# Kernel optimization log

Measured on AMD Instinct MI355X. Metric: run time of the kernel, lower is better.

Reference implementation:

```python
import jax, jax.numpy as jnp
import numpy as np

N_NODES = 50000
N_EDGES = 800000
IN_DIM = 100
HIDDEN = 16
N_CLASSES = 40


def setup_inputs() -> dict:
    key = jax.random.key(0)
    k1, k2, k3, k4, k5, k6 = jax.random.split(key, 6)
    features = jax.random.normal(k1, (N_NODES, IN_DIM), dtype=jnp.float32)
    edge_src = jax.random.randint(k2, (N_EDGES,), 0, N_NODES, dtype=jnp.int32)
    edge_dst = jax.random.randint(k3, (N_EDGES,), 0, N_NODES, dtype=jnp.int32)
    edge_vals = jax.random.uniform(k4, (N_EDGES,), dtype=jnp.float32)
    W1 = jax.random.uniform(k5, (IN_DIM, HIDDEN), dtype=jnp.float32)
    W2 = jax.random.uniform(k6, (HIDDEN, N_CLASSES), dtype=jnp.float32)
    return {"features": features, "edge_src": edge_src, "edge_dst": edge_dst,
            "edge_vals": edge_vals, "W1": W1, "W2": W2}


def _spmm(edge_src, edge_dst, edge_vals, x):
    # z = A @ x with A given as (dst, src, val) edge list; equivalent to the
    # partition-loop addmm accumulation in broadcast().
    msgs = edge_vals[:, None] * x[edge_src]            # [E, d]
    return jax.ops.segment_sum(msgs, edge_dst, num_segments=x.shape[0])


def reference(features, edge_src, edge_dst, edge_vals, W1, W2):
    h = jax.nn.relu(_spmm(edge_src, edge_dst, edge_vals, features) @ W1)  # [N, 16]
    out = _spmm(edge_src, edge_dst, edge_vals, h) @ W2                    # [N, C]
    return jax.nn.log_softmax(out, axis=1)
```

## Files before the change

kernel.cpp:

```cpp
#include <hip/hip_runtime.h>

#define N_NODES   50000
#define N_EDGES   800000
#define IN_DIM    100
#define HIDDEN    16
#define N_CLASSES 40

#define BSHIFT 6
#define NPB    64
#define NBKT   782
#define PB     256
#define EPB    3125
#define EPT    7
#define CAP    2048
#define GNODES 32
#define GEMMB  782

#define K1_LDS 33456

__global__ __launch_bounds__(512) void build_and_gemm(const int* __restrict__ src,
                                                      const int* __restrict__ dst,
                                                      const float* __restrict__ val,
                                                      const float* __restrict__ X,
                                                      const float* __restrict__ W,
                                                      int* __restrict__ BTt,
                                                      int2* __restrict__ binned,
                                                      float* __restrict__ Y) {
    __shared__ __align__(16) char smem[K1_LDS];
    const int tid = threadIdx.x;

    if (blockIdx.x < PB) {
        int*  cnt    = (int*)smem;
        int*  lcur   = (int*)(smem + 3200);
        int*  sd     = (int*)(smem + 6400);
        int2* staged = (int2*)(smem + 8448);
        const int b = blockIdx.x, e0 = b * EPB;

        for (int k = tid; k < NBKT; k += 512) cnt[k] = 0;
        __syncthreads();

        int pk[EPT], ps[EPT]; float pv[EPT];
#pragma unroll
        for (int q = 0; q < EPT; ++q) {
            const int i = tid + q * 512;
            if (i < EPB) {
                const int e = e0 + i;
                const int d = dst[e];
                pk[q] = d >> BSHIFT;
                ps[q] = src[e] | ((d & (NPB - 1)) << 16);
                pv[q] = val[e];
                atomicAdd(&cnt[pk[q]], 1);
            } else pk[q] = -1;
        }
        __syncthreads();

        const int k0 = 2 * tid, k1 = 2 * tid + 1;
        const int a  = (k0 < NBKT) ? cnt[k0] : 0;
        const int bb = (k1 < NBKT) ? cnt[k1] : 0;
        const int s  = a + bb;
        sd[tid] = s;
        __syncthreads();
        for (int off = 1; off < 512; off <<= 1) {
            const int u = (tid >= off) ? sd[tid - off] : 0;
            __syncthreads();
            sd[tid] += u;
            __syncthreads();
        }
        const int excl = sd[tid] - s;
        if (k0 < NBKT) { lcur[k0] = excl;     BTt[k0 * PB + b] = excl; }
        if (k1 < NBKT) { lcur[k1] = excl + a; BTt[k1 * PB + b] = excl + a; }
        if (tid == 0)  BTt[NBKT * PB + b] = EPB;
        __syncthreads();

#pragma unroll
        for (int q = 0; q < EPT; ++q) {
            if (pk[q] >= 0) {
                const int pos = atomicAdd(&lcur[pk[q]], 1);
                staged[pos] = make_int2(ps[q], __float_as_int(pv[q]));
            }
        }
        __syncthreads();

        for (int i = tid; i < EPB; i += 512)
            binned[e0 + i] = staged[i];
    } else {
        float* sX = (float*)smem;
        float* sW = (float*)(smem + 25600);
        const int b2   = blockIdx.x - PB;
        const int row0 = b2 * 64;
        const int nrows = min(64, N_NODES - row0);

        const float4* W4 = (const float4*)W;
        float4* sW4 = (float4*)sW;
        for (int i = tid; i < (IN_DIM * HIDDEN) / 4; i += 512) sW4[i] = W4[i];
        const float4* X4 = (const float4*)(X + (size_t)row0 * IN_DIM);
        float4* sX4 = (float4*)sX;
        const int nf4 = nrows * (IN_DIM / 4);
        for (int i = tid; i < nf4; i += 512) sX4[i] = X4[i];
        __syncthreads();

        const int r = tid >> 3, hh = tid & 7;
        if (r >= nrows) return;
        float2 acc = make_float2(0.f, 0.f);
        const float* xr = &sX[r * IN_DIM];
#pragma unroll
        for (int k = 0; k < IN_DIM; ++k) {
            const float xk = xr[k];
            const float2 w = *(const float2*)&sW[k * HIDDEN + hh * 2];
            acc.x = fmaf(xk, w.x, acc.x);
            acc.y = fmaf(xk, w.y, acc.y);
        }
        *(float2*)&Y[(size_t)(row0 + r) * HIDDEN + hh * 2] = acc;
    }
}

__global__ __launch_bounds__(256) void sort_gather(const int* __restrict__ BTt,
                                                   const int2* __restrict__ binned,
                                                   const float* __restrict__ Xin,
                                                   int2* __restrict__ sorted,
                                                   int2* __restrict__ meta,
                                                   float* __restrict__ Z) {
    __shared__ int2 raw[CAP];
    __shared__ int2 srt[CAP];
    __shared__ int  cnt[NPB];
    __shared__ int  cur[NPB];
    __shared__ int  wsum[4];
    const int tid = threadIdx.x, k = blockIdx.x;
    const int lane = tid & 63, w = tid >> 6;

    if (tid < NPB) cnt[tid] = 0;

    const int rs = BTt[k * PB + tid];
    const int re = BTt[(k + 1) * PB + tid];
    const int len = re - rs;
    int x = len;
#pragma unroll
    for (int d = 1; d < 64; d <<= 1) {
        const int y = __shfl_up(x, d, 64);
        if (lane >= d) x += y;
    }
    if (lane == 63) wsum[w] = x;
    __syncthreads();
    int add = 0;
    for (int i = 0; i < w; ++i) add += wsum[i];
    const int tot = wsum[0] + wsum[1] + wsum[2] + wsum[3];

    int o = add + x - len;
    const int2* rb = binned + (size_t)tid * EPB;
    for (int p = rs; p < re; ++p, ++o) raw[o] = rb[p];
    __syncthreads();

    for (int i = tid; i < tot; i += 256)
        atomicAdd(&cnt[(raw[i].x >> 16) & (NPB - 1)], 1);
    __syncthreads();

    if (tid < NPB) {
        const int v  = cnt[tid];
        const int vp = (v + 1) & ~1;
        int xx = vp;
#pragma unroll
        for (int d = 1; d < 64; d <<= 1) {
            const int y = __shfl_up(xx, d, 64);
            if (tid >= d) xx += y;
        }
        const int excl = xx - vp;
        cur[tid] = excl;
        const int node = k * NPB + tid;
        if (node < N_NODES) meta[node] = make_int2(k * CAP + excl, v);
        if (tid == NPB - 1) wsum[0] = xx;
    }
    __syncthreads();
    const int padTot = wsum[0];

    for (int i = tid; i < tot; i += 256) {
        const int2 e = raw[i];
        const int pos = atomicAdd(&cur[(e.x >> 16) & (NPB - 1)], 1);
        srt[pos] = make_int2(e.x & 0xFFFF, e.y);
    }
    __syncthreads();

    for (int i = tid; i < padTot; i += 256)
        sorted[(size_t)k * CAP + i] = srt[i];

    const int g = tid >> 2, q = tid & 3;
    const int node = k * NPB + g;
    if (node >= N_NODES) return;
    const int deg = cnt[g];
    const int beg = cur[g] - deg;
    const float4* X4 = (const float4*)Xin;
    float4 acc = make_float4(0.f, 0.f, 0.f, 0.f);
    for (int p = beg; p < beg + deg; ++p) {
        const int2 e = srt[p];
        const float v = __int_as_float(e.y);
        const float4 xv = X4[(size_t)e.x * 4 + q];
        acc.x = fmaf(v, xv.x, acc.x);
        acc.y = fmaf(v, xv.y, acc.y);
        acc.z = fmaf(v, xv.z, acc.z);
        acc.w = fmaf(v, xv.w, acc.w);
    }
    acc.x = fmaxf(acc.x, 0.f); acc.y = fmaxf(acc.y, 0.f);
    acc.z = fmaxf(acc.z, 0.f); acc.w = fmaxf(acc.w, 0.f);
    ((float4*)Z)[(size_t)node * 4 + q] = acc;
}

__global__ __launch_bounds__(256) void gather_out(const int2* __restrict__ meta,
                                                  const int2* __restrict__ sorted,
                                                  const float* __restrict__ X,
                                                  const float* __restrict__ W2,
                                                  float* __restrict__ out) {
    __shared__ float sW[HIDDEN * N_CLASSES];
    __shared__ float zt[GNODES * 17];
    const int tid = threadIdx.x;
    for (int i = tid; i < HIDDEN * N_CLASSES; i += 256) sW[i] = W2[i];

    const int g = tid >> 3, j = tid & 7;
    const int n = blockIdx.x * GNODES + g;

    float2 acc = make_float2(0.f, 0.f);
    if (n < N_NODES) {
        const int2 md = meta[n];
        const int beg = md.x, end = md.x + md.y;
        const float2* X2 = (const float2*)X;
        int p = beg;
        for (; p + 4 <= end; p += 4) {
            const int4 ea = *(const int4*)&sorted[p];
            const int4 eb = *(const int4*)&sorted[p + 2];
            const float2 x0 = X2[(size_t)ea.x * 8 + j];
            const float2 x1 = X2[(size_t)ea.z * 8 + j];
            const float2 x2 = X2[(size_t)eb.x * 8 + j];
            const float2 x3 = X2[(size_t)eb.z * 8 + j];
            const float v0 = __int_as_float(ea.y), v1 = __int_as_float(ea.w);
            const float v2 = __int_as_float(eb.y), v3 = __int_as_float(eb.w);
            acc.x = fmaf(v0, x0.x, acc.x); acc.y = fmaf(v0, x0.y, acc.y);
            acc.x = fmaf(v1, x1.x, acc.x); acc.y = fmaf(v1, x1.y, acc.y);
            acc.x = fmaf(v2, x2.x, acc.x); acc.y = fmaf(v2, x2.y, acc.y);
            acc.x = fmaf(v3, x3.x, acc.x); acc.y = fmaf(v3, x3.y, acc.y);
        }
        for (; p < end; ++p) {
            const int2 e = sorted[p];
            const float2 xv = X2[(size_t)e.x * 8 + j];
            const float v = __int_as_float(e.y);
            acc.x = fmaf(v, xv.x, acc.x); acc.y = fmaf(v, xv.y, acc.y);
        }
    }
    zt[g * 17 + j * 2]     = acc.x;
    zt[g * 17 + j * 2 + 1] = acc.y;
    __syncthreads();
    if (n >= N_NODES) return;

    float z[HIDDEN];
#pragma unroll
    for (int k = 0; k < HIDDEN; ++k) z[k] = zt[g * 17 + k];

    float o[5];
#pragma unroll
    for (int i = 0; i < 5; ++i) o[i] = 0.f;
#pragma unroll
    for (int k = 0; k < HIDDEN; ++k) {
        const float zk = z[k];
#pragma unroll
        for (int i = 0; i < 5; ++i)
            o[i] = fmaf(zk, sW[k * N_CLASSES + j * 5 + i], o[i]);
    }

    float m = o[0];
#pragma unroll
    for (int i = 1; i < 5; ++i) m = fmaxf(m, o[i]);
#pragma unroll
    for (int d = 1; d < 8; d <<= 1) m = fmaxf(m, __shfl_xor(m, d, 8));
    float se = 0.f;
#pragma unroll
    for (int i = 0; i < 5; ++i) se += __expf(o[i] - m);
#pragma unroll
    for (int d = 1; d < 8; d <<= 1) se += __shfl_xor(se, d, 8);
    const float lse = m + __logf(se);

    float* orow = out + (size_t)n * N_CLASSES + j * 5;
#pragma unroll
    for (int i = 0; i < 5; ++i) orow[i] = o[i] - lse;
}

extern "C" void kernel_launch(void* const* d_in, const int* in_sizes, int n_in,
                              void* d_out, int out_size, void* d_ws, size_t ws_size,
                              hipStream_t stream) {
    const float* features = (const float*)d_in[0];
    const int*   edge_src = (const int*)d_in[1];
    const int*   edge_dst = (const int*)d_in[2];
    const float* edge_val = (const float*)d_in[3];
    const float* W1       = (const float*)d_in[4];
    const float* W2       = (const float*)d_in[5];
    float*       out      = (float*)d_out;

    char* base = (char*)d_ws;
    const size_t HNB = (size_t)N_NODES * HIDDEN * sizeof(float);
    float* y1     = (float*)(base);
    float* z1     = (float*)(base + HNB);
    int2*  binned = (int2*) (base + 2 * HNB);
    int2*  sortd  = (int2*) (base + 2 * HNB + (size_t)N_EDGES * 8);
    char*  tail   = base + 2 * HNB + (size_t)N_EDGES * 8
                         + (size_t)NBKT * CAP * 8;
    int*   BTt    = (int*) (tail);
    int2*  meta   = (int2*)(tail + (((size_t)(NBKT + 1) * PB * 4 + 255) & ~255ULL));

    build_and_gemm<<<PB + GEMMB, 512, 0, stream>>>(edge_src, edge_dst, edge_val,
                                                   features, W1, BTt, binned, y1);
    sort_gather<<<NBKT, 256, 0, stream>>>(BTt, binned, y1, sortd, meta, z1);
    gather_out<<<(N_NODES + GNODES - 1) / GNODES, 256, 0, stream>>>(meta, sortd, z1, W2, out);
}
```

Baseline: 125.6 us.

## Replace per-bucket counting sort with LDS atomic accumulation for both SpMM layers

Drops the second-level counting sort and the sorted/meta arrays. Each bucket block now reads its raw edges, and 16 lanes per edge accumulate v*x into a shared-memory accumulator with float atomics. The output layer reuses the same bucketed edge stream instead of re-reading a globally stored sorted list. The block-level prefix scan in the build kernel is also replaced with a wavefront shuffle scan. This removes the sort passes and the global writes and reads of the sorted edges, at the cost of LDS atomic contention and non-deterministic summation order.

Result: slower. 283.4 us (+125.7%).

```diff
diff --git a/kernel.cpp b/kernel.cpp
--- a/kernel.cpp
+++ b/kernel.cpp
@@ -13,7 +13,6 @@
 #define EPB    3125
 #define EPT    7
 #define CAP    2048
-#define GNODES 32
 #define GEMMB  782
 
 #define K1_LDS 33456
@@ -32,9 +31,10 @@
     if (blockIdx.x < PB) {
         int*  cnt    = (int*)smem;
         int*  lcur   = (int*)(smem + 3200);
-        int*  sd     = (int*)(smem + 6400);
+        int*  wpre   = (int*)(smem + 6400);
         int2* staged = (int2*)(smem + 8448);
         const int b = blockIdx.x, e0 = b * EPB;
+        const int lane = tid & 63, w = tid >> 6;
 
         for (int k = tid; k < NBKT; k += 512) cnt[k] = 0;
         __syncthreads();
@@ -58,15 +58,17 @@
         const int a  = (k0 < NBKT) ? cnt[k0] : 0;
         const int bb = (k1 < NBKT) ? cnt[k1] : 0;
         const int s  = a + bb;
-        sd[tid] = s;
-        __syncthreads();
-        for (int off = 1; off < 512; off <<= 1) {
-            const int u = (tid >= off) ? sd[tid - off] : 0;
-            __syncthreads();
-            sd[tid] += u;
-            __syncthreads();
-        }
-        const int excl = sd[tid] - s;
+        int x = s;
+#pragma unroll
+        for (int d = 1; d < 64; d <<= 1) {
+            const int y = __shfl_up(x, d, 64);
+            if (lane >= d) x += y;
+        }
+        if (lane == 63) wpre[w] = x;
+        __syncthreads();
+        int add = 0;
+        for (int i = 0; i < w; ++i) add += wpre[i];
+        const int excl = add + x - s;
         if (k0 < NBKT) { lcur[k0] = excl;     BTt[k0 * PB + b] = excl; }
         if (k1 < NBKT) { lcur[k1] = excl + a; BTt[k1 * PB + b] = excl + a; }
         if (tid == 0)  BTt[NBKT * PB + b] = EPB;
@@ -106,29 +108,30 @@
 #pragma unroll
         for (int k = 0; k < IN_DIM; ++k) {
             const float xk = xr[k];
-            const float2 w = *(const float2*)&sW[k * HIDDEN + hh * 2];
-            acc.x = fmaf(xk, w.x, acc.x);
-            acc.y = fmaf(xk, w.y, acc.y);
+            const float2 wv = *(const float2*)&sW[k * HIDDEN + hh * 2];
+            acc.x = fmaf(xk, wv.x, acc.x);
+            acc.y = fmaf(xk, wv.y, acc.y);
         }
         *(float2*)&Y[(size_t)(row0 + r) * HIDDEN + hh * 2] = acc;
     }
 }
 
-__global__ __launch_bounds__(256) void sort_gather(const int* __restrict__ BTt,
-                                                   const int2* __restrict__ binned,
-                                                   const float* __restrict__ Xin,
-                                                   int2* __restrict__ sorted,
-                                                   int2* __restrict__ meta,
-                                                   float* __restrict__ Z) {
-    __shared__ int2 raw[CAP];
-    __shared__ int2 srt[CAP];
-    __shared__ int  cnt[NPB];
-    __shared__ int  cur[NPB];
-    __shared__ int  wsum[4];
+template <bool IS_OUT>
+__global__ __launch_bounds__(256) void spmm_bucket2(const int* __restrict__ BTt,
+                                                    const int2* __restrict__ binned,
+                                                    const float* __restrict__ X,
+                                                    const float* __restrict__ W2,
+                                                    float* __restrict__ outp) {
+    __shared__ int2  raw[CAP];
+    __shared__ float acc[NPB * HIDDEN];
+    __shared__ int   wpre[4];
+    __shared__ float sW[HIDDEN * N_CLASSES];
     const int tid = threadIdx.x, k = blockIdx.x;
     const int lane = tid & 63, w = tid >> 6;
 
-    if (tid < NPB) cnt[tid] = 0;
+    for (int i = tid; i < NPB * HIDDEN; i += 256) acc[i] = 0.f;
+    if (IS_OUT)
+        for (int i = tid; i < HIDDEN * N_CLASSES; i += 256) sW[i] = W2[i];
 
     const int rs = BTt[k * PB + tid];
     const int re = BTt[(k + 1) * PB + tid];
@@ -139,145 +142,66 @@
         const int y = __shfl_up(x, d, 64);
         if (lane >= d) x += y;
     }
-    if (lane == 63) wsum[w] = x;
+    if (lane == 63) wpre[w] = x;
     __syncthreads();
     int add = 0;
-    for (int i = 0; i < w; ++i) add += wsum[i];
-    const int tot = wsum[0] + wsum[1] + wsum[2] + wsum[3];
+    for (int i = 0; i < w; ++i) add += wpre[i];
+    const int tot = wpre[0] + wpre[1] + wpre[2] + wpre[3];
 
     int o = add + x - len;
     const int2* rb = binned + (size_t)tid * EPB;
     for (int p = rs; p < re; ++p, ++o) raw[o] = rb[p];
     __syncthreads();
 
-    for (int i = tid; i < tot; i += 256)
-        atomicAdd(&cnt[(raw[i].x >> 16) & (NPB - 1)], 1);
+    const int j = tid & 15;
+    for (int i = tid >> 4; i < tot; i += 16) {
+        const int2 e = raw[i];
+        const int  sn = e.x & 0xFFFF;
+        const int  n  = (e.x >> 16) & (NPB - 1);
+        const float v = __int_as_float(e.y);
+        const float xv = X[(size_t)sn * HIDDEN + j];
+        unsafeAtomicAdd(&acc[n * HIDDEN + j], v * xv);
+    }
     __syncthreads();
 
-    if (tid < NPB) {
-        const int v  = cnt[tid];
-        const int vp = (v + 1) & ~1;
-        int xx = vp;
-#pragma unroll
-        for (int d = 1; d < 64; d <<= 1) {
-            const int y = __shfl_up(xx, d, 64);
-            if (tid >= d) xx += y;
-        }
-        const int excl = xx - vp;
-        cur[tid] = excl;
-        const int node = k * NPB + tid;
-        if (node < N_NODES) meta[node] = make_int2(k * CAP + excl, v);
-        if (tid == NPB - 1) wsum[0] = xx;
-    }
-    __syncthreads();
-    const int padTot = wsum[0];
-
-    for (int i = tid; i < tot; i += 256) {
-        const int2 e = raw[i];
-        const int pos = atomicAdd(&cur[(e.x >> 16) & (NPB - 1)], 1);
-        srt[pos] = make_int2(e.x & 0xFFFF, e.y);
-    }
-    __syncthreads();
-
-    for (int i = tid; i < padTot; i += 256)
-        sorted[(size_t)k * CAP + i] = srt[i];
-
-    const int g = tid >> 2, q = tid & 3;
-    const int node = k * NPB + g;
-    if (node >= N_NODES) return;
-    const int deg = cnt[g];
-    const int beg = cur[g] - deg;
-    const float4* X4 = (const float4*)Xin;
-    float4 acc = make_float4(0.f, 0.f, 0.f, 0.f);
-    for (int p = beg; p < beg + deg; ++p) {
-        const int2 e = srt[p];
-        const float v = __int_as_float(e.y);
-        const float4 xv = X4[(size_t)e.x * 4 + q];
-        acc.x = fmaf(v, xv.x, acc.x);
-        acc.y = fmaf(v, xv.y, acc.y);
-        acc.z = fmaf(v, xv.z, acc.z);
-        acc.w = fmaf(v, xv.w, acc.w);
-    }
-    acc.x = fmaxf(acc.x, 0.f); acc.y = fmaxf(acc.y, 0.f);
-    acc.z = fmaxf(acc.z, 0.f); acc.w = fmaxf(acc.w, 0.f);
-    ((float4*)Z)[(size_t)node * 4 + q] = acc;
-}
-
-__global__ __launch_bounds__(256) void gather_out(const int2* __restrict__ meta,
-                                                  const int2* __restrict__ sorted,
-                                                  const float* __restrict__ X,
-                                                  const float* __restrict__ W2,
-                                                  float* __restrict__ out) {
-    __shared__ float sW[HIDDEN * N_CLASSES];
-    __shared__ float zt[GNODES * 17];
-    const int tid = threadIdx.x;
-    for (int i = tid; i < HIDDEN * N_CLASSES; i += 256) sW[i] = W2[i];
-
-    const int g = tid >> 3, j = tid & 7;
-    const int n = blockIdx.x * GNODES + g;
-
-    float2 acc = make_float2(0.f, 0.f);
-    if (n < N_NODES) {
-        const int2 md = meta[n];
-        const int beg = md.x, end = md.x + md.y;
-        const float2* X2 = (const float2*)X;
-        int p = beg;
-        for (; p + 4 <= end; p += 4) {
-            const int4 ea = *(const int4*)&sorted[p];
-            const int4 eb = *(const int4*)&sorted[p + 2];
-            const float2 x0 = X2[(size_t)ea.x * 8 + j];
-            const float2 x1 = X2[(size_t)ea.z * 8 + j];
-            const float2 x2 = X2[(size_t)eb.x * 8 + j];
-            const float2 x3 = X2[(size_t)eb.z * 8 + j];
-            const float v0 = __int_as_float(ea.y), v1 = __int_as_float(ea.w);
-            const float v2 = __int_as_float(eb.y), v3 = __int_as_float(eb.w);
-            acc.x = fmaf(v0, x0.x, acc.x); acc.y = fmaf(v0, x0.y, acc.y);
-            acc.x = fmaf(v1, x1.x, acc.x); acc.y = fmaf(v1, x1.y, acc.y);
-            acc.x = fmaf(v2, x2.x, acc.x); acc.y = fmaf(v2, x2.y, acc.y);
-            acc.x = fmaf(v3, x3.x, acc.x); acc.y = fmaf(v3, x3.y, acc.y);
-        }
-        for (; p < end; ++p) {
-            const int2 e = sorted[p];
-            const float2 xv = X2[(size_t)e.x * 8 + j];
-            const float v = __int_as_float(e.y);
-            acc.x = fmaf(v, xv.x, acc.x); acc.y = fmaf(v, xv.y, acc.y);
-        }
-    }
-    zt[g * 17 + j * 2]     = acc.x;
-    zt[g * 17 + j * 2 + 1] = acc.y;
-    __syncthreads();
-    if (n >= N_NODES) return;
-
-    float z[HIDDEN];
-#pragma unroll
-    for (int k = 0; k < HIDDEN; ++k) z[k] = zt[g * 17 + k];
-
-    float o[5];
-#pragma unroll
-    for (int i = 0; i < 5; ++i) o[i] = 0.f;
-#pragma unroll
-    for (int k = 0; k < HIDDEN; ++k) {
-        const float zk = z[k];
-#pragma unroll
-        for (int i = 0; i < 5; ++i)
-            o[i] = fmaf(zk, sW[k * N_CLASSES + j * 5 + i], o[i]);
-    }
-
-    float m = o[0];
-#pragma unroll
-    for (int i = 1; i < 5; ++i) m = fmaxf(m, o[i]);
-#pragma unroll
-    for (int d = 1; d < 8; d <<= 1) m = fmaxf(m, __shfl_xor(m, d, 8));
-    float se = 0.f;
-#pragma unroll
-    for (int i = 0; i < 5; ++i) se += __expf(o[i] - m);
-#pragma unroll
-    for (int d = 1; d < 8; d <<= 1) se += __shfl_xor(se, d, 8);
-    const float lse = m + __logf(se);
-
-    float* orow = out + (size_t)n * N_CLASSES + j * 5;
-#pragma unroll
-    for (int i = 0; i < 5; ++i) orow[i] = o[i] - lse;
+    if (!IS_OUT) {
+        const int node = k * NPB + (tid >> 2);
+        if (node >= N_NODES) return;
+        float4 o4 = *(const float4*)&acc[tid * 4];
+        o4.x = fmaxf(o4.x, 0.f); o4.y = fmaxf(o4.y, 0.f);
+        o4.z = fmaxf(o4.z, 0.f); o4.w = fmaxf(o4.w, 0.f);
+        ((float4*)outp)[(size_t)node * 4 + (tid & 3)] = o4;
+    } else {
+        const int g = tid >> 2, q = tid & 3;
+        const int n = k * NPB + g;
+        if (n >= N_NODES) return;
+        float oc[10];
+#pragma unroll
+        for (int c = 0; c < 10; ++c) oc[c] = 0.f;
+        const float* zr = &acc[g * HIDDEN];
+#pragma unroll
+        for (int kk = 0; kk < HIDDEN; ++kk) {
+            const float zk = zr[kk];
+            const float* wr = &sW[kk * N_CLASSES + q * 10];
+#pragma unroll
+            for (int c = 0; c < 10; ++c) oc[c] = fmaf(zk, wr[c], oc[c]);
+        }
+        float m = oc[0];
+#pragma unroll
+        for (int c = 1; c < 10; ++c) m = fmaxf(m, oc[c]);
+#pragma unroll
+        for (int d = 1; d < 4; d <<= 1) m = fmaxf(m, __shfl_xor(m, d, 4));
+        float se = 0.f;
+#pragma unroll
+        for (int c = 0; c < 10; ++c) se += __expf(oc[c] - m);
+#pragma unroll
+        for (int d = 1; d < 4; d <<= 1) se += __shfl_xor(se, d, 4);
+        const float lse = m + __logf(se);
+
+        float* orow = outp + (size_t)n * N_CLASSES + q * 10;
+#pragma unroll
+        for (int c = 0; c < 10; ++c) orow[c] = oc[c] - lse;
+    }
 }
 
 extern "C" void kernel_launch(void* const* d_in, const int* in_sizes, int n_in,
@@ -296,14 +220,10 @@
     float* y1     = (float*)(base);
     float* z1     = (float*)(base + HNB);
     int2*  binned = (int2*) (base + 2 * HNB);
-    int2*  sortd  = (int2*) (base + 2 * HNB + (size_t)N_EDGES * 8);
-    char*  tail   = base + 2 * HNB + (size_t)N_EDGES * 8
-                         + (size_t)NBKT * CAP * 8;
-    int*   BTt    = (int*) (tail);
-    int2*  meta   = (int2*)(tail + (((size_t)(NBKT + 1) * PB * 4 + 255) & ~255ULL));
+    int*   BTt    = (int*)  (base + 2 * HNB + (size_t)N_EDGES * 8);
 
     build_and_gemm<<<PB + GEMMB, 512, 0, stream>>>(edge_src, edge_dst, edge_val,
                                                    features, W1, BTt, binned, y1);
-    sort_gather<<<NBKT, 256, 0, stream>>>(BTt, binned, y1, sortd, meta, z1);
-    gather_out<<<(N_NODES + GNODES - 1) / GNODES, 256, 0, stream>>>(meta, sortd, z1, W2, out);
+    spmm_bucket2<false><<<NBKT, 256, 0, stream>>>(BTt, binned, y1, nullptr, z1);
+    spmm_bucket2<true><<<NBKT, 256, 0, stream>>>(BTt, binned, z1, W2, out);
 }
```

## Use smaller binning blocks, warp-shuffle scan, and read binned edges directly in sort

Applied to the files above, without the earlier changes.

The edge-binning phase now runs 500 blocks of 256 threads over 1600 edges each instead of 256 blocks of 512, and the GEMM part uses 32-row tiles. The per-block bucket prefix sum moves from a shared-memory Hillis-Steele scan with many barriers to a wave-shuffle scan. sort_gather no longer stages raw edges in LDS; each thread reads its partition slices from global memory twice, for counting and for scattering, and the gather loop is unrolled by two. The aim is better occupancy and fewer barriers, at the cost of re-reading binned data from global memory and more BTt entries per bucket.

Measured after the change: 129.7 us. 3.3% more time.

```diff
diff --git a/kernel.cpp b/kernel.cpp
--- a/kernel.cpp
+++ b/kernel.cpp
@@ -9,16 +9,17 @@
 #define BSHIFT 6
 #define NPB    64
 #define NBKT   782
-#define PB     256
-#define EPB    3125
+#define PB     500
+#define EPB    1600
 #define EPT    7
 #define CAP    2048
+#define GROWS  32
+#define GEMMB  1563
 #define GNODES 32
-#define GEMMB  782
-
-#define K1_LDS 33456
-
-__global__ __launch_bounds__(512) void build_and_gemm(const int* __restrict__ src,
+
+#define K1_LDS 19264
+
+__global__ __launch_bounds__(256) void build_and_gemm(const int* __restrict__ src,
                                                       const int* __restrict__ dst,
                                                       const float* __restrict__ val,
                                                       const float* __restrict__ X,
@@ -32,17 +33,18 @@
     if (blockIdx.x < PB) {
         int*  cnt    = (int*)smem;
         int*  lcur   = (int*)(smem + 3200);
-        int*  sd     = (int*)(smem + 6400);
-        int2* staged = (int2*)(smem + 8448);
+        int*  wpre   = (int*)(smem + 6400);
+        int2* staged = (int2*)(smem + 6464);
         const int b = blockIdx.x, e0 = b * EPB;
-
-        for (int k = tid; k < NBKT; k += 512) cnt[k] = 0;
+        const int lane = tid & 63, w = tid >> 6;
+
+        for (int k = tid; k < NBKT; k += 256) cnt[k] = 0;
         __syncthreads();
 
         int pk[EPT], ps[EPT]; float pv[EPT];
 #pragma unroll
         for (int q = 0; q < EPT; ++q) {
-            const int i = tid + q * 512;
+            const int i = tid + q * 256;
             if (i < EPB) {
                 const int e = e0 + i;
                 const int d = dst[e];
@@ -54,22 +56,34 @@
         }
         __syncthreads();
 
-        const int k0 = 2 * tid, k1 = 2 * tid + 1;
-        const int a  = (k0 < NBKT) ? cnt[k0] : 0;
-        const int bb = (k1 < NBKT) ? cnt[k1] : 0;
-        const int s  = a + bb;
-        sd[tid] = s;
-        __syncthreads();
-        for (int off = 1; off < 512; off <<= 1) {
-            const int u = (tid >= off) ? sd[tid - off] : 0;
-            __syncthreads();
-            sd[tid] += u;
-            __syncthreads();
-        }
-        const int excl = sd[tid] - s;
-        if (k0 < NBKT) { lcur[k0] = excl;     BTt[k0 * PB + b] = excl; }
-        if (k1 < NBKT) { lcur[k1] = excl + a; BTt[k1 * PB + b] = excl + a; }
-        if (tid == 0)  BTt[NBKT * PB + b] = EPB;
+        int c[4], s = 0;
+#pragma unroll
+        for (int u = 0; u < 4; ++u) {
+            const int kk = 4 * tid + u;
+            c[u] = (kk < NBKT) ? cnt[kk] : 0;
+            s += c[u];
+        }
+        int x = s;
+#pragma unroll
+        for (int d = 1; d < 64; d <<= 1) {
+            const int y = __shfl_up(x, d, 64);
+            if (lane >= d) x += y;
+        }
+        if (lane == 63) wpre[w] = x;
+        __syncthreads();
+        int add = 0;
+        for (int i = 0; i < w; ++i) add += wpre[i];
+        int run = add + x - s;
+#pragma unroll
+        for (int u = 0; u < 4; ++u) {
+            const int kk = 4 * tid + u;
+            if (kk < NBKT) {
+                lcur[kk] = run;
+                BTt[kk * PB + b] = run;
+                run += c[u];
+            }
+        }
+        if (tid == 0) BTt[NBKT * PB + b] = EPB;
         __syncthreads();
 
 #pragma unroll
@@ -81,22 +95,22 @@
         }
         __syncthreads();
 
-        for (int i = tid; i < EPB; i += 512)
+        for (int i = tid; i < EPB; i += 256)
             binned[e0 + i] = staged[i];
     } else {
         float* sX = (float*)smem;
-        float* sW = (float*)(smem + 25600);
+        float* sW = (float*)(smem + 12800);
         const int b2   = blockIdx.x - PB;
-        const int row0 = b2 * 64;
-        const int nrows = min(64, N_NODES - row0);
+        const int row0 = b2 * GROWS;
+        const int nrows = min(GROWS, N_NODES - row0);
 
         const float4* W4 = (const float4*)W;
         float4* sW4 = (float4*)sW;
-        for (int i = tid; i < (IN_DIM * HIDDEN) / 4; i += 512) sW4[i] = W4[i];
+        for (int i = tid; i < (IN_DIM * HIDDEN) / 4; i += 256) sW4[i] = W4[i];
         const float4* X4 = (const float4*)(X + (size_t)row0 * IN_DIM);
         float4* sX4 = (float4*)sX;
         const int nf4 = nrows * (IN_DIM / 4);
-        for (int i = tid; i < nf4; i += 512) sX4[i] = X4[i];
+        for (int i = tid; i < nf4; i += 256) sX4[i] = X4[i];
         __syncthreads();
 
         const int r = tid >> 3, hh = tid & 7;
@@ -104,11 +118,11 @@
         float2 acc = make_float2(0.f, 0.f);
         const float* xr = &sX[r * IN_DIM];
 #pragma unroll
-        for (int k = 0; k < IN_DIM; ++k) {
-            const float xk = xr[k];
-            const float2 w = *(const float2*)&sW[k * HIDDEN + hh * 2];
-            acc.x = fmaf(xk, w.x, acc.x);
-            acc.y = fmaf(xk, w.y, acc.y);
+        for (int kk = 0; kk < IN_DIM; ++kk) {
+            const float xk = xr[kk];
+            const float2 wv = *(const float2*)&sW[kk * HIDDEN + hh * 2];
+            acc.x = fmaf(xk, wv.x, acc.x);
+            acc.y = fmaf(xk, wv.y, acc.y);
         }
         *(float2*)&Y[(size_t)(row0 + r) * HIDDEN + hh * 2] = acc;
     }
@@ -120,65 +134,59 @@
                                                    int2* __restrict__ sorted,
                                                    int2* __restrict__ meta,
                                                    float* __restrict__ Z) {
-    __shared__ int2 raw[CAP];
     __shared__ int2 srt[CAP];
     __shared__ int  cnt[NPB];
     __shared__ int  cur[NPB];
-    __shared__ int  wsum[4];
+    __shared__ int  sPad;
     const int tid = threadIdx.x, k = blockIdx.x;
-    const int lane = tid & 63, w = tid >> 6;
 
     if (tid < NPB) cnt[tid] = 0;
 
-    const int rs = BTt[k * PB + tid];
-    const int re = BTt[(k + 1) * PB + tid];
-    const int len = re - rs;
-    int x = len;
-#pragma unroll
-    for (int d = 1; d < 64; d <<= 1) {
-        const int y = __shfl_up(x, d, 64);
-        if (lane >= d) x += y;
-    }
-    if (lane == 63) wsum[w] = x;
-    __syncthreads();
-    int add = 0;
-    for (int i = 0; i < w; ++i) add += wsum[i];
-    const int tot = wsum[0] + wsum[1] + wsum[2] + wsum[3];
-
-    int o = add + x - len;
-    const int2* rb = binned + (size_t)tid * EPB;
-    for (int p = rs; p < re; ++p, ++o) raw[o] = rb[p];
-    __syncthreads();
-
-    for (int i = tid; i < tot; i += 256)
-        atomicAdd(&cnt[(raw[i].x >> 16) & (NPB - 1)], 1);
+    const int rs0 = BTt[k * PB + tid];
+    const int re0 = BTt[(k + 1) * PB + tid];
+    const int rr1 = tid + 256;
+    int rs1 = 0, re1 = 0;
+    if (rr1 < PB) { rs1 = BTt[k * PB + rr1]; re1 = BTt[(k + 1) * PB + rr1]; }
+    __syncthreads();
+
+    for (int p = rs0; p < re0; ++p)
+        atomicAdd(&cnt[(binned[(size_t)tid * EPB + p].x >> 16) & (NPB - 1)], 1);
+    if (rr1 < PB)
+        for (int p = rs1; p < re1; ++p)
+            atomicAdd(&cnt[(binned[(size_t)rr1 * EPB + p].x >> 16) & (NPB - 1)], 1);
     __syncthreads();
 
     if (tid < NPB) {
         const int v  = cnt[tid];
         const int vp = (v + 1) & ~1;
-        int xx = vp;
+        int x = vp;
 #pragma unroll
         for (int d = 1; d < 64; d <<= 1) {
-            const int y = __shfl_up(xx, d, 64);
-            if (tid >= d) xx += y;
-        }
-        const int excl = xx - vp;
+            const int y = __shfl_up(x, d, 64);
+            if (tid >= d) x += y;
+        }
+        const int excl = x - vp;
         cur[tid] = excl;
         const int node = k * NPB + tid;
         if (node < N_NODES) meta[node] = make_int2(k * CAP + excl, v);
-        if (tid == NPB - 1) wsum[0] = xx;
-    }
-    __syncthreads();
-    const int padTot = wsum[0];
-
-    for (int i = tid; i < tot; i += 256) {
-        const int2 e = raw[i];
+        if (tid == NPB - 1) sPad = x;
+    }
+    __syncthreads();
+
+    for (int p = rs0; p < re0; ++p) {
+        const int2 e = binned[(size_t)tid * EPB + p];
         const int pos = atomicAdd(&cur[(e.x >> 16) & (NPB - 1)], 1);
         srt[pos] = make_int2(e.x & 0xFFFF, e.y);
     }
-    __syncthreads();
-
+    if (rr1 < PB)
+        for (int p = rs1; p < re1; ++p) {
+            const int2 e = binned[(size_t)rr1 * EPB + p];
+            const int pos = atomicAdd(&cur[(e.x >> 16) & (NPB - 1)], 1);
+            srt[pos] = make_int2(e.x & 0xFFFF, e.y);
+        }
+    __syncthreads();
+
+    const int padTot = sPad;
     for (int i = tid; i < padTot; i += 256)
         sorted[(size_t)k * CAP + i] = srt[i];
 
@@ -189,14 +197,25 @@
     const int beg = cur[g] - deg;
     const float4* X4 = (const float4*)Xin;
     float4 acc = make_float4(0.f, 0.f, 0.f, 0.f);
-    for (int p = beg; p < beg + deg; ++p) {
+    int p = beg;
+    for (; p + 2 <= beg + deg; p += 2) {
+        const int2 e0 = srt[p];
+        const int2 e1 = srt[p + 1];
+        const float v0 = __int_as_float(e0.y);
+        const float v1 = __int_as_float(e1.y);
+        const float4 x0 = X4[(size_t)e0.x * 4 + q];
+        const float4 x1 = X4[(size_t)e1.x * 4 + q];
+        acc.x = fmaf(v0, x0.x, acc.x); acc.y = fmaf(v0, x0.y, acc.y);
+        acc.z = fmaf(v0, x0.z, acc.z); acc.w = fmaf(v0, x0.w, acc.w);
+        acc.x = fmaf(v1, x1.x, acc.x); acc.y = fmaf(v1, x1.y, acc.y);
+        acc.z = fmaf(v1, x1.z, acc.z); acc.w = fmaf(v1, x1.w, acc.w);
+    }
+    if (p < beg + deg) {
         const int2 e = srt[p];
         const float v = __int_as_float(e.y);
         const float4 xv = X4[(size_t)e.x * 4 + q];
-        acc.x = fmaf(v, xv.x, acc.x);
-        acc.y = fmaf(v, xv.y, acc.y);
-        acc.z = fmaf(v, xv.z, acc.z);
-        acc.w = fmaf(v, xv.w, acc.w);
+        acc.x = fmaf(v, xv.x, acc.x); acc.y = fmaf(v, xv.y, acc.y);
+        acc.z = fmaf(v, xv.z, acc.z); acc.w = fmaf(v, xv.w, acc.w);
     }
     acc.x = fmaxf(acc.x, 0.f); acc.y = fmaxf(acc.y, 0.f);
     acc.z = fmaxf(acc.z, 0.f); acc.w = fmaxf(acc.w, 0.f);
@@ -302,7 +321,7 @@
     int*   BTt    = (int*) (tail);
     int2*  meta   = (int2*)(tail + (((size_t)(NBKT + 1) * PB * 4 + 255) & ~255ULL));
 
-    build_and_gemm<<<PB + GEMMB, 512, 0, stream>>>(edge_src, edge_dst, edge_val,
+    build_and_gemm<<<PB + GEMMB, 256, 0, stream>>>(edge_src, edge_dst, edge_val,
                                                    features, W1, BTt, binned, y1);
     sort_gather<<<NBKT, 256, 0, stream>>>(BTt, binned, y1, sortd, meta, z1);
     gather_out<<<(N_NODES + GNODES - 1) / GNODES, 256, 0, stream>>>(meta, sortd, z1, W2, out);
```
